# Kernel tuning notes

Hardware: AMD Instinct MI355X
Metric: run time of the kernel (lower is better)

Reference implementation:

```python
import jax, jax.numpy as jnp
import numpy as np

jax.config.update("jax_enable_x64", True)

# config
B, S = 4, 4096
H_SIZE = 2048          # hidden_size
VOCAB = 128000         # engram_base_vocab_size
MAX_NGRAM = 3          # engram_max_ngram_size -> orders 2..3
PRIME = 500009         # engram_n_embed_per_ngram (same prime for every order)
N_HEAD = 4             # engram_n_head_per_ngram
E = 32                 # engram_embed_dim
KS = 4                 # short conv kernel size
NUM_ORDERS = MAX_NGRAM - 1
TOTAL_HEADS = NUM_ORDERS * N_HEAD
TOTAL_ROWS = PRIME * N_HEAD * NUM_ORDERS  # flat multi-head table rows


def setup_inputs() -> dict:
    key = jax.random.key(0)
    k_ids, k_h, k_tab, k_cw, k_hp, k_gp, k_op = jax.random.split(key, 7)
    input_ids = jax.random.randint(k_ids, (B, S), 0, VOCAB, dtype=jnp.int64)
    hidden_states = jax.random.normal(k_h, (B, S, H_SIZE), dtype=jnp.float32)
    # identity compressed-tokenizer mapping buffer
    mapping = jnp.arange(VOCAB, dtype=jnp.int64)
    # deterministic odd multipliers, seeded like _build_multipliers
    rng = np.random.default_rng(0 * 10007 + 0 * 1009)
    mults = rng.integers(1, 2 ** 31, size=(NUM_ORDERS, N_HEAD, MAX_NGRAM))
    multipliers = jnp.asarray(mults * 2 + 1, dtype=jnp.int64)
    table = 0.02 * jax.random.normal(k_tab, (TOTAL_ROWS, E), dtype=jnp.float32)
    conv_w = 0.1 * jax.random.normal(k_cw, (E, KS), dtype=jnp.float32)  # depthwise taps
    conv_b = jnp.zeros((E,), dtype=jnp.float32)
    Wh = 0.05 * jax.random.normal(k_hp, (E, TOTAL_HEADS * E), dtype=jnp.float32)
    Wg = 0.02 * jax.random.normal(k_gp, (E, H_SIZE), dtype=jnp.float32)
    Wo = 0.02 * jax.random.normal(k_op, (H_SIZE, E), dtype=jnp.float32)
    return {"input_ids": input_ids, "hidden_states": hidden_states,
            "mapping": mapping, "multipliers": multipliers, "table": table,
            "conv_w": conv_w, "conv_b": conv_b, "Wh": Wh, "Wg": Wg, "Wo": Wo}


def _hash_indices(compressed, multipliers):
    """XOR-mix n-gram hash indices -> [B, S, TOTAL_HEADS] int64."""
    all_idx = []
    offset = 0
    for oi, k in enumerate(range(2, MAX_NGRAM + 1)):
        # forward sliding window, clamped at last token (matches cat/expand trick)
        pos = jnp.minimum(jnp.arange(S)[:, None] + jnp.arange(k)[None, :], S - 1)  # [S,k]
        ng = compressed[:, pos]                                  # [B,S,k]
        m = multipliers[oi, :, :k]                               # [nh,k]
        prod = ng[:, :, None, :] * m[None, None, :, :]           # [B,S,nh,k]
        h = prod[..., 0]
        for p in range(1, k):
            h = h ^ prod[..., p]
        idx = h % PRIME + (offset + jnp.arange(N_HEAD, dtype=jnp.int64) * PRIME)
        all_idx.append(idx)
        offset += PRIME * N_HEAD
    return jnp.concatenate(all_idx, axis=-1)


def reference(input_ids, hidden_states, mapping, multipliers, table,
              conv_w, conv_b, Wh, Wg, Wo):
    compressed = mapping[input_ids]                              # [B,S]
    indices = _hash_indices(compressed, multipliers)             # [B,S,TOTAL_HEADS]
    emb = table[indices].reshape(B, S, TOTAL_HEADS * E)          # multi-head gather
    emb = emb @ Wh.T                                             # head_proj -> [B,S,E]
    # causal depthwise short conv (kernel KS, left pad KS-1)
    xp = jnp.pad(emb, ((0, 0), (KS - 1, 0), (0, 0)))
    emb = sum(xp[:, j:j + S, :] * conv_w[:, j] for j in range(KS)) + conv_b
    gate = jax.nn.sigmoid(hidden_states @ Wg.T)                  # [B,S,E]
    return (gate * emb) @ Wo.T                                   # [B,S,H_SIZE]
```

## Files before the change

kernel.cpp:

```cpp
#include <hip/hip_runtime.h>
#include <hip/hip_bf16.h>
#include <stdint.h>

#define HSZ 2048
#define PRIME 500009u
#define CHUNK 128
#define NCH 16

typedef __attribute__((ext_vector_type(8))) short short8;
typedef __attribute__((ext_vector_type(4))) float f32x4;
typedef __attribute__((ext_vector_type(4))) unsigned uint4v;
typedef __attribute__((ext_vector_type(2))) unsigned uint2v;

#define MEMFENCE asm volatile("" ::: "memory")
#define BARRIER() do { MEMFENCE; __builtin_amdgcn_s_barrier(); MEMFENCE; } while (0)
#define WAIT_LGKM0 asm volatile("s_waitcnt lgkmcnt(0)" ::: "memory")
#define WAIT_VM(n) asm volatile("s_waitcnt vmcnt(" #n ")" ::: "memory")

__device__ __forceinline__ unsigned pk2(float x, float y) {
  __hip_bfloat162 h = __float22bfloat162_rn(make_float2(x, y));
  return *reinterpret_cast<unsigned*>(&h);
}
__device__ __forceinline__ short f2bf(float f) {
  __hip_bfloat16 h = __float2bfloat16(f);
  return *reinterpret_cast<short*>(&h);
}
__device__ __forceinline__ short8 pack8(float4 a, float4 b) {
  uint4v u = {pk2(a.x, a.y), pk2(a.z, a.w), pk2(b.x, b.y), pk2(b.z, b.w)};
  return __builtin_bit_cast(short8, u);
}
__device__ __forceinline__ short8 load8_bf(const float* __restrict__ p) {
  float4 a = *reinterpret_cast<const float4*>(p);
  float4 b = *reinterpret_cast<const float4*>(p + 4);
  return pack8(a, b);
}
__device__ __forceinline__ void gload_lds16(const float* g, void* l) {
  __builtin_amdgcn_global_load_lds(
      (const __attribute__((address_space(1))) void*)g,
      (__attribute__((address_space(3))) void*)l, 16, 0, 0);
}

__global__ __launch_bounds__(256, 2) void engram_fused(
    const int* __restrict__ ids, const int* __restrict__ mapping,
    const unsigned* __restrict__ mult, const float* __restrict__ table,
    const float* __restrict__ Wh, const float* __restrict__ hidden,
    const float* __restrict__ cw, const float* __restrict__ cb,
    const float* __restrict__ Wg, const float* __restrict__ Wo,
    float* __restrict__ out) {
  __shared__ __align__(16) float hbuf[2][32][CHUNK];
  __shared__ __align__(16) short A_lds[48][264];
  __shared__ __align__(16) float emb48[48][36];
  __shared__ float emb_c[32][33];
  __shared__ __align__(16) short ge_lds[32][40];
  __shared__ int idx_lds[384];

  const int tid = threadIdx.x;
  const int wid = tid >> 6, lane = tid & 63;
  const int l16 = lane & 15, q = lane >> 4;
  const int t0 = blockIdx.x * 32;

  auto STAGE = [&](int buf, int kc) {
#pragma unroll
    for (int j = 0; j < 4; ++j) {
      int r0 = wid * 8 + j * 2;
      int r = r0 + (lane >> 5);
      unsigned cf = (((unsigned)(lane & 31) * 16u) ^ (((unsigned)r & 7u) << 4)) >> 2;
      const float* src = hidden + (size_t)(t0 + r) * HSZ + kc * CHUNK + cf;
      gload_lds16(src, &hbuf[buf][r0][0]);
    }
  };

#pragma unroll
  for (int p = 0; p < 2; ++p) {
    int hh = p * 256 + tid;
    if (hh < 384) {
      int slot = hh >> 3, head = hh & 7;
      int tg = t0 - 16 + slot;
      if (tg < 0) tg = 0;
      int b = tg >> 12, s = tg & 4095;
      const int* idb = ids + (b << 12);
      int s1 = s + 1 > 4095 ? 4095 : s + 1;
      int s2 = s + 2 > 4095 ? 4095 : s + 2;
      uint64_t c0 = (unsigned)mapping[idb[s]];
      uint64_t c1 = (unsigned)mapping[idb[s1]];
      uint64_t c2 = (unsigned)mapping[idb[s2]];
      int mb = head * 3;
      uint64_t h = (c0 * (uint64_t)mult[mb]) ^ (c1 * (uint64_t)mult[mb + 1]);
      if (head >= 4) h ^= c2 * (uint64_t)mult[mb + 2];
      idx_lds[hh] = (int)((unsigned)(h % PRIME) + (unsigned)head * PRIME);
    }
  }

  STAGE(0, 0);
  STAGE(1, 1);

  WAIT_LGKM0; BARRIER();

#pragma unroll
  for (int p = 0; p < 12; ++p) {
    int r = p * 32 + (tid >> 3);
    int c4 = (tid & 7) * 4;
    int row = idx_lds[r];
    float4 v = *reinterpret_cast<const float4*>(table + (size_t)row * 32 + c4);
    uint2v pk = {pk2(v.x, v.y), pk2(v.z, v.w)};
    *reinterpret_cast<uint2v*>(&A_lds[r >> 3][(r & 7) * 32 + c4]) = pk;
  }
  WAIT_LGKM0; BARRIER();

  for (int job = wid; job < 6; job += 4) {
    int jt = job >> 1, e0 = (job & 1) * 16;
    f32x4 acc = {0.f, 0.f, 0.f, 0.f};
#pragma unroll
    for (int ks = 0; ks < 8; ++ks) {
      short8 wf = load8_bf(Wh + (size_t)(e0 + l16) * 256 + ks * 32 + q * 8);
      short8 a = *reinterpret_cast<const short8*>(&A_lds[jt * 16 + l16][ks * 32 + q * 8]);
      acc = __builtin_amdgcn_mfma_f32_16x16x32_bf16(wf, a, acc, 0, 0, 0);
    }
    *reinterpret_cast<f32x4*>(&emb48[jt * 16 + l16][e0 + q * 4]) = acc;
  }
  WAIT_LGKM0; BARRIER();

#pragma unroll
  for (int it = 0; it < 4; ++it) {
    int ii = it * 256 + tid;
    int tl = ii >> 5, e = ii & 31;
    int s = (t0 & 4095) + tl;
    float a = cb[e];
#pragma unroll
    for (int j = 0; j < 4; ++j)
      if (s - 3 + j >= 0) a += cw[e * 4 + j] * emb48[13 + tl + j][e];
    emb_c[tl][e] = a;
  }
  WAIT_LGKM0; BARRIER();

  const int tt = wid >> 1, ee = wid & 1;
  const int R = tt * 16 + l16;
  const unsigned sw = ((unsigned)R & 7u) << 4;
  const char* hb0 = (const char*)&hbuf[0][R][0];
  const char* hb1 = (const char*)&hbuf[1][R][0];
  const float* wgp = Wg + (size_t)(ee * 16 + l16) * HSZ + q * 8;
  f32x4 acc = {0.f, 0.f, 0.f, 0.f};

  for (int kc = 0; kc < NCH - 1; ++kc) {
    WAIT_VM(12);
    BARRIER();
    const char* hb = (kc & 1) ? hb1 : hb0;
    short8 A[4], B[4];
#pragma unroll
    for (int ks = 0; ks < 4; ++ks) {
      unsigned x0 = (unsigned)(ks * 128 + q * 32);
      float4 a0 = *reinterpret_cast<const float4*>(hb + (x0 ^ sw));
      float4 a1 = *reinterpret_cast<const float4*>(hb + ((x0 + 16) ^ sw));
      A[ks] = pack8(a0, a1);
      B[ks] = load8_bf(wgp + kc * CHUNK + ks * 32);
    }
    WAIT_LGKM0;
    BARRIER();
    if (kc < NCH - 2) STAGE(kc & 1, kc + 2);
#pragma unroll
    for (int ks = 0; ks < 4; ++ks)
      acc = __builtin_amdgcn_mfma_f32_16x16x32_bf16(A[ks], B[ks], acc, 0, 0, 0);
  }
  {
    WAIT_VM(0);
    BARRIER();
#pragma unroll
    for (int ks = 0; ks < 4; ++ks) {
      unsigned x0 = (unsigned)(ks * 128 + q * 32);
      float4 a0 = *reinterpret_cast<const float4*>(hb1 + (x0 ^ sw));
      float4 a1 = *reinterpret_cast<const float4*>(hb1 + ((x0 + 16) ^ sw));
      short8 B0 = load8_bf(wgp + (NCH - 1) * CHUNK + ks * 32);
      acc = __builtin_amdgcn_mfma_f32_16x16x32_bf16(pack8(a0, a1), B0, acc, 0, 0, 0);
    }
  }

#pragma unroll
  for (int j = 0; j < 4; ++j) {
    int r = tt * 16 + q * 4 + j, c = ee * 16 + l16;
    float g = 1.f / (1.f + __expf(-acc[j]));
    ge_lds[r][c] = f2bf(g * emb_c[r][c]);
  }
  WAIT_LGKM0; BARRIER();

  short8 Af0 = *reinterpret_cast<const short8*>(&ge_lds[l16][q * 8]);
  short8 Af1 = *reinterpret_cast<const short8*>(&ge_lds[16 + l16][q * 8]);
  float* orow0 = out + (size_t)(t0 + l16) * HSZ;
  float* orow1 = out + (size_t)(t0 + 16 + l16) * HSZ;
  int hbase = wid * 512;
#pragma unroll 8
  for (int ht = 0; ht < 32; ++ht) {
    int h0 = hbase + ht * 16;
    short8 aw = load8_bf(Wo + (size_t)(h0 + l16) * 32 + q * 8);
    f32x4 z = {0.f, 0.f, 0.f, 0.f};
    f32x4 o0 = __builtin_amdgcn_mfma_f32_16x16x32_bf16(aw, Af0, z, 0, 0, 0);
    f32x4 o1 = __builtin_amdgcn_mfma_f32_16x16x32_bf16(aw, Af1, z, 0, 0, 0);
    *reinterpret_cast<f32x4*>(orow0 + h0 + q * 4) = o0;
    *reinterpret_cast<f32x4*>(orow1 + h0 + q * 4) = o1;
  }
}

extern "C" void kernel_launch(void* const* d_in, const int* in_sizes, int n_in,
                              void* d_out, int out_size, void* d_ws, size_t ws_size,
                              hipStream_t stream) {
  const int* ids = (const int*)d_in[0];
  const float* hidden = (const float*)d_in[1];
  const int* mapping = (const int*)d_in[2];
  const unsigned* mult = (const unsigned*)d_in[3];
  const float* table = (const float*)d_in[4];
  const float* cw = (const float*)d_in[5];
  const float* cb = (const float*)d_in[6];
  const float* Wh = (const float*)d_in[7];
  const float* Wg = (const float*)d_in[8];
  const float* Wo = (const float*)d_in[9];
  float* out = (float*)d_out;

  engram_fused<<<512, 256, 0, stream>>>(ids, mapping, mult, table, Wh, hidden,
                                        cw, cb, Wg, Wo, out);
}
```

Baseline: 92.55 us.

## Split gate GEMM into two 16-token halves and overlap output stores with second half

The hidden-state gate projection now runs in two passes of 16 tokens each. Wg chunks are staged into LDS alongside hidden, and the K dimension is split across warp pairs, with partial sums reduced through LDS. The output projection and stores for the first 16 tokens are interleaved with the second pass's gate GEMM, so output write bandwidth overlaps with hidden-state streaming. The cost is more barriers per chunk, smaller chunks, and extra LDS for the Wg buffers and the reduction scratch, which may lower occupancy.

Result: slower. 103.7 us (+12.1%).

```diff
diff --git a/kernel.cpp b/kernel.cpp
--- a/kernel.cpp
+++ b/kernel.cpp
@@ -4,8 +4,8 @@
 
 #define HSZ 2048
 #define PRIME 500009u
-#define CHUNK 128
-#define NCH 16
+#define CHUNK 64
+#define NCH 32
 
 typedef __attribute__((ext_vector_type(8))) short short8;
 typedef __attribute__((ext_vector_type(4))) float f32x4;
@@ -47,11 +47,13 @@
     const float* __restrict__ cw, const float* __restrict__ cb,
     const float* __restrict__ Wg, const float* __restrict__ Wo,
     float* __restrict__ out) {
-  __shared__ __align__(16) float hbuf[2][32][CHUNK];
+  __shared__ __align__(16) float hbuf[2][16][CHUNK];
+  __shared__ __align__(16) float wgbuf[2][32][CHUNK];
   __shared__ __align__(16) short A_lds[48][264];
   __shared__ __align__(16) float emb48[48][36];
   __shared__ float emb_c[32][33];
   __shared__ __align__(16) short ge_lds[32][40];
+  __shared__ float accred[2][4][64];
   __shared__ int idx_lds[384];
 
   const int tid = threadIdx.x;
@@ -59,16 +61,25 @@
   const int l16 = lane & 15, q = lane >> 4;
   const int t0 = blockIdx.x * 32;
 
-  auto STAGE = [&](int buf, int kc) {
-#pragma unroll
-    for (int j = 0; j < 4; ++j) {
-      int r0 = wid * 8 + j * 2;
-      int r = r0 + (lane >> 5);
-      unsigned cf = (((unsigned)(lane & 31) * 16u) ^ (((unsigned)r & 7u) << 4)) >> 2;
-      const float* src = hidden + (size_t)(t0 + r) * HSZ + kc * CHUNK + cf;
-      gload_lds16(src, &hbuf[buf][r0][0]);
+  auto STAGE = [&](int buf, int kc, int ro) {
+    {
+      int r0 = wid * 4;
+      int r = r0 + (lane >> 4);
+      unsigned c4 = (((unsigned)l16 * 16u) ^ (((unsigned)r & 7u) << 4)) >> 2;
+      gload_lds16(hidden + (size_t)(t0 + ro + r) * HSZ + kc * CHUNK + c4,
+                  &hbuf[buf][r0][0]);
+    }
+#pragma unroll
+    for (int j = 0; j < 2; ++j) {
+      int r0 = wid * 8 + j * 4;
+      int r = r0 + (lane >> 4);
+      unsigned c4 = (((unsigned)l16 * 16u) ^ (((unsigned)r & 7u) << 4)) >> 2;
+      gload_lds16(Wg + (size_t)r * HSZ + kc * CHUNK + c4, &wgbuf[buf][r0][0]);
     }
   };
+
+  STAGE(0, 0, 0);
+  STAGE(1, 1, 0);
 
 #pragma unroll
   for (int p = 0; p < 2; ++p) {
@@ -90,10 +101,6 @@
       idx_lds[hh] = (int)((unsigned)(h % PRIME) + (unsigned)head * PRIME);
     }
   }
-
-  STAGE(0, 0);
-  STAGE(1, 1);
-
   WAIT_LGKM0; BARRIER();
 
 #pragma unroll
@@ -133,69 +140,131 @@
   }
   WAIT_LGKM0; BARRIER();
 
-  const int tt = wid >> 1, ee = wid & 1;
-  const int R = tt * 16 + l16;
-  const unsigned sw = ((unsigned)R & 7u) << 4;
-  const char* hb0 = (const char*)&hbuf[0][R][0];
-  const char* hb1 = (const char*)&hbuf[1][R][0];
-  const float* wgp = Wg + (size_t)(ee * 16 + l16) * HSZ + q * 8;
-  f32x4 acc = {0.f, 0.f, 0.f, 0.f};
-
-  for (int kc = 0; kc < NCH - 1; ++kc) {
-    WAIT_VM(12);
+  const int ee = wid & 1, kh = wid >> 1;
+  const unsigned swA = ((unsigned)l16 & 7u) << 4;
+  const int Rb = ee * 16 + l16;
+  const unsigned swB = ((unsigned)Rb & 7u) << 4;
+  const unsigned x0 = (unsigned)(kh * 128 + q * 32);
+  const char* hA0 = (const char*)&hbuf[0][l16][0];
+  const char* hA1 = (const char*)&hbuf[1][l16][0];
+  const char* wB0 = (const char*)&wgbuf[0][Rb][0];
+  const char* wB1 = (const char*)&wgbuf[1][Rb][0];
+  f32x4 z = {0.f, 0.f, 0.f, 0.f};
+
+  f32x4 accA = {0.f, 0.f, 0.f, 0.f};
+  for (int kc = 0; kc < 31; ++kc) {
+    WAIT_VM(3);
     BARRIER();
-    const char* hb = (kc & 1) ? hb1 : hb0;
-    short8 A[4], B[4];
-#pragma unroll
-    for (int ks = 0; ks < 4; ++ks) {
-      unsigned x0 = (unsigned)(ks * 128 + q * 32);
-      float4 a0 = *reinterpret_cast<const float4*>(hb + (x0 ^ sw));
-      float4 a1 = *reinterpret_cast<const float4*>(hb + ((x0 + 16) ^ sw));
-      A[ks] = pack8(a0, a1);
-      B[ks] = load8_bf(wgp + kc * CHUNK + ks * 32);
-    }
-    WAIT_LGKM0;
+    const char* hb = (kc & 1) ? hA1 : hA0;
+    const char* wb = (kc & 1) ? wB1 : wB0;
+    float4 a0 = *reinterpret_cast<const float4*>(hb + (x0 ^ swA));
+    float4 a1 = *reinterpret_cast<const float4*>(hb + ((x0 + 16) ^ swA));
+    float4 b0 = *reinterpret_cast<const float4*>(wb + (x0 ^ swB));
+    float4 b1 = *reinterpret_cast<const float4*>(wb + ((x0 + 16) ^ swB));
+    short8 A = pack8(a0, a1), B = pack8(b0, b1);
+    WAIT_LGKM0; BARRIER();
+    if (kc < 30) STAGE(kc & 1, kc + 2, 0);
+    accA = __builtin_amdgcn_mfma_f32_16x16x32_bf16(A, B, accA, 0, 0, 0);
+  }
+  {
+    WAIT_VM(0); BARRIER();
+    float4 a0 = *reinterpret_cast<const float4*>(hA1 + (x0 ^ swA));
+    float4 a1 = *reinterpret_cast<const float4*>(hA1 + ((x0 + 16) ^ swA));
+    float4 b0 = *reinterpret_cast<const float4*>(wB1 + (x0 ^ swB));
+    float4 b1 = *reinterpret_cast<const float4*>(wB1 + ((x0 + 16) ^ swB));
+    accA = __builtin_amdgcn_mfma_f32_16x16x32_bf16(pack8(a0, a1), pack8(b0, b1), accA, 0, 0, 0);
+  }
+
+  if (kh == 1) {
+#pragma unroll
+    for (int j = 0; j < 4; ++j) accred[ee][j][lane] = accA[j];
+  }
+  WAIT_LGKM0; BARRIER();
+  short8 wo_cur = load8_bf(Wo + (size_t)(wid * 512 + l16) * 32 + q * 8);
+  STAGE(0, 0, 16);
+  STAGE(1, 1, 16);
+  if (kh == 0) {
+#pragma unroll
+    for (int j = 0; j < 4; ++j) {
+      float s = accA[j] + accred[ee][j][lane];
+      int r = q * 4 + j, c = ee * 16 + l16;
+      float g = 1.f / (1.f + __expf(-s));
+      ge_lds[r][c] = f2bf(g * emb_c[r][c]);
+    }
+  }
+  WAIT_LGKM0; BARRIER();
+  short8 AfA = *reinterpret_cast<const short8*>(&ge_lds[l16][q * 8]);
+  float* orowA = out + (size_t)(t0 + l16) * HSZ;
+
+  f32x4 accB = {0.f, 0.f, 0.f, 0.f};
+  {
+    WAIT_VM(3); BARRIER();
+    float4 a0 = *reinterpret_cast<const float4*>(hA0 + (x0 ^ swA));
+    float4 a1 = *reinterpret_cast<const float4*>(hA0 + ((x0 + 16) ^ swA));
+    float4 b0 = *reinterpret_cast<const float4*>(wB0 + (x0 ^ swB));
+    float4 b1 = *reinterpret_cast<const float4*>(wB0 + ((x0 + 16) ^ swB));
+    short8 A = pack8(a0, a1), B = pack8(b0, b1);
+    WAIT_LGKM0; BARRIER();
+    f32x4 o = __builtin_amdgcn_mfma_f32_16x16x32_bf16(wo_cur, AfA, z, 0, 0, 0);
+    *reinterpret_cast<f32x4*>(orowA + wid * 512 + q * 4) = o;
+    wo_cur = load8_bf(Wo + (size_t)(wid * 512 + 16 + l16) * 32 + q * 8);
+    STAGE(0, 2, 16);
+    accB = __builtin_amdgcn_mfma_f32_16x16x32_bf16(A, B, accB, 0, 0, 0);
+  }
+  for (int kc = 1; kc <= 30; ++kc) {
+    WAIT_VM(6);
     BARRIER();
-    if (kc < NCH - 2) STAGE(kc & 1, kc + 2);
-#pragma unroll
-    for (int ks = 0; ks < 4; ++ks)
-      acc = __builtin_amdgcn_mfma_f32_16x16x32_bf16(A[ks], B[ks], acc, 0, 0, 0);
+    const char* hb = (kc & 1) ? hA1 : hA0;
+    const char* wb = (kc & 1) ? wB1 : wB0;
+    float4 a0 = *reinterpret_cast<const float4*>(hb + (x0 ^ swA));
+    float4 a1 = *reinterpret_cast<const float4*>(hb + ((x0 + 16) ^ swA));
+    float4 b0 = *reinterpret_cast<const float4*>(wb + (x0 ^ swB));
+    float4 b1 = *reinterpret_cast<const float4*>(wb + ((x0 + 16) ^ swB));
+    short8 A = pack8(a0, a1), B = pack8(b0, b1);
+    WAIT_LGKM0; BARRIER();
+    f32x4 o = __builtin_amdgcn_mfma_f32_16x16x32_bf16(wo_cur, AfA, z, 0, 0, 0);
+    *reinterpret_cast<f32x4*>(orowA + wid * 512 + kc * 16 + q * 4) = o;
+    wo_cur = load8_bf(Wo + (size_t)(wid * 512 + (kc + 1) * 16 + l16) * 32 + q * 8);
+    if (kc < 30) STAGE(kc & 1, kc + 2, 16);
+    accB = __builtin_amdgcn_mfma_f32_16x16x32_bf16(A, B, accB, 0, 0, 0);
   }
   {
-    WAIT_VM(0);
-    BARRIER();
-#pragma unroll
-    for (int ks = 0; ks < 4; ++ks) {
-      unsigned x0 = (unsigned)(ks * 128 + q * 32);
-      float4 a0 = *reinterpret_cast<const float4*>(hb1 + (x0 ^ sw));
-      float4 a1 = *reinterpret_cast<const float4*>(hb1 + ((x0 + 16) ^ sw));
-      short8 B0 = load8_bf(wgp + (NCH - 1) * CHUNK + ks * 32);
-      acc = __builtin_amdgcn_mfma_f32_16x16x32_bf16(pack8(a0, a1), B0, acc, 0, 0, 0);
-    }
-  }
-
-#pragma unroll
-  for (int j = 0; j < 4; ++j) {
-    int r = tt * 16 + q * 4 + j, c = ee * 16 + l16;
-    float g = 1.f / (1.f + __expf(-acc[j]));
-    ge_lds[r][c] = f2bf(g * emb_c[r][c]);
-  }
-  WAIT_LGKM0; BARRIER();
-
-  short8 Af0 = *reinterpret_cast<const short8*>(&ge_lds[l16][q * 8]);
-  short8 Af1 = *reinterpret_cast<const short8*>(&ge_lds[16 + l16][q * 8]);
-  float* orow0 = out + (size_t)(t0 + l16) * HSZ;
-  float* orow1 = out + (size_t)(t0 + 16 + l16) * HSZ;
-  int hbase = wid * 512;
-#pragma unroll 8
+    WAIT_VM(3); BARRIER();
+    float4 a0 = *reinterpret_cast<const float4*>(hA1 + (x0 ^ swA));
+    float4 a1 = *reinterpret_cast<const float4*>(hA1 + ((x0 + 16) ^ swA));
+    float4 b0 = *reinterpret_cast<const float4*>(wB1 + (x0 ^ swB));
+    float4 b1 = *reinterpret_cast<const float4*>(wB1 + ((x0 + 16) ^ swB));
+    short8 A = pack8(a0, a1), B = pack8(b0, b1);
+    WAIT_LGKM0; BARRIER();
+    f32x4 o = __builtin_amdgcn_mfma_f32_16x16x32_bf16(wo_cur, AfA, z, 0, 0, 0);
+    *reinterpret_cast<f32x4*>(orowA + wid * 512 + 31 * 16 + q * 4) = o;
+    accB = __builtin_amdgcn_mfma_f32_16x16x32_bf16(A, B, accB, 0, 0, 0);
+  }
+
+  if (kh == 1) {
+#pragma unroll
+    for (int j = 0; j < 4; ++j) accred[ee][j][lane] = accB[j];
+  }
+  WAIT_LGKM0; BARRIER();
+  if (kh == 0) {
+#pragma unroll
+    for (int j = 0; j < 4; ++j) {
+      float s = accB[j] + accred[ee][j][lane];
+      int r = q * 4 + j, c = ee * 16 + l16;
+      float g = 1.f / (1.f + __expf(-s));
+      ge_lds[16 + r][c] = f2bf(g * emb_c[16 + r][c]);
+    }
+  }
+  WAIT_LGKM0; BARRIER();
+
+  short8 AfB = *reinterpret_cast<const short8*>(&ge_lds[16 + l16][q * 8]);
+  float* orowB = out + (size_t)(t0 + 16 + l16) * HSZ;
+#pragma unroll 4
   for (int ht = 0; ht < 32; ++ht) {
-    int h0 = hbase + ht * 16;
+    int h0 = wid * 512 + ht * 16;
     short8 aw = load8_bf(Wo + (size_t)(h0 + l16) * 32 + q * 8);
-    f32x4 z = {0.f, 0.f, 0.f, 0.f};
-    f32x4 o0 = __builtin_amdgcn_mfma_f32_16x16x32_bf16(aw, Af0, z, 0, 0, 0);
-    f32x4 o1 = __builtin_amdgcn_mfma_f32_16x16x32_bf16(aw, Af1, z, 0, 0, 0);
-    *reinterpret_cast<f32x4*>(orow0 + h0 + q * 4) = o0;
-    *reinterpret_cast<f32x4*>(orow1 + h0 + q * 4) = o1;
+    f32x4 o = __builtin_amdgcn_mfma_f32_16x16x32_bf16(aw, AfB, z, 0, 0, 0);
+    *reinterpret_cast<f32x4*>(orowB + h0 + q * 4) = o;
   }
 }
 
```
